# Kernel tuning notes

Hardware: AMD Instinct MI355X
Metric: run time of the kernel (lower is better)

The kernel has to match this reference:

```python
import jax, jax.numpy as jnp
import numpy as np

V, H, B, T = 512, 1024, 128, 128
N_STACK = 4      # n_control_stack = n_work_stack = 4
N_OUT = 4        # n_out_sym
ISIN = 4         # isinstance_dim
ZERO_OFF = 1e-6  # self.zero_offset


def _norm(x):
    n = jnp.linalg.norm(x, axis=-1, keepdims=True)
    return x / jnp.maximum(n, 1e-12)


def nl(x, W):
    # NormalizedLinear: L2-normalize input rows and weight rows, then linear (no bias)
    return _norm(x) @ _norm(W).T


def stack_pop(S, p):
    # hard pop: read at pointer, move pointer down; stack contents unchanged
    read = jnp.einsum('bnv,bn->bv', S, p)
    return read, jnp.roll(p, -1, axis=1)


def stack_hard_push(S, p, v):
    p2 = jnp.roll(p, 1, axis=1)
    S2 = S * (1.0 - p2[..., None]) + v[:, None, :] * p2[..., None]
    return S2, p2


def stack_soft_op(S, p, sharpen, push, pop, nop, val):
    # NTM-style blended push/pop/noop followed by pointer sharpening w^g / sum(w^g)
    p_push = jnp.roll(p, 1, axis=1)
    S_push = S * (1.0 - p_push[..., None]) + val[:, None, :] * p_push[..., None]
    p_pop = jnp.roll(p, -1, axis=1)
    new_p = push[:, None] * p_push + pop[:, None] * p_pop + nop[:, None] * p
    new_S = push[:, None, None] * S_push + (pop + nop)[:, None, None] * S
    sp = jnp.maximum(new_p, 0.0) ** sharpen
    new_p = sp / (sp.sum(axis=1, keepdims=True) + 1e-12)
    return new_S, new_p


def setup_inputs() -> dict:
    key = jax.random.key(0)
    ks = jax.random.split(key, 24)
    sv = 1.0 / np.sqrt(V)
    sh = 1.0 / np.sqrt(H)
    si = 1.0 / np.sqrt(ISIN)
    d = {}
    d['x'] = jax.random.normal(ks[0], (B, T, V), jnp.float32)
    d['W_isin1'] = jax.random.normal(ks[1], (ISIN, V), jnp.float32) * sv
    d['W_isin2'] = jax.random.normal(ks[2], (V, ISIN), jnp.float32) * si
    # 3 gate heads per stack (push, pop, null), stacked on leading axis
    d['cop_W1'] = jax.random.normal(ks[3], (3, H, V), jnp.float32) * sv
    d['cop_b1'] = jax.random.normal(ks[4], (3, H), jnp.float32) * sv
    d['cop_W2'] = jax.random.normal(ks[5], (3, H), jnp.float32) * sh
    d['cop_b2'] = jax.random.normal(ks[6], (3,), jnp.float32) * sh
    d['wop_W1'] = jax.random.normal(ks[7], (3, H, V), jnp.float32) * sv
    d['wop_b1'] = jax.random.normal(ks[8], (3, H), jnp.float32) * sv
    d['wop_W2'] = jax.random.normal(ks[9], (3, H), jnp.float32) * sh
    d['wop_b2'] = jax.random.normal(ks[10], (3,), jnp.float32) * sh
    d['ctrl_W1'] = jax.random.normal(ks[11], (H, V), jnp.float32) * sv
    d['ctrl_W2'] = jax.random.normal(ks[12], (V, H), jnp.float32) * sh
    d['work_W1'] = jax.random.normal(ks[13], (H, V), jnp.float32) * sv
    d['work_W2'] = jax.random.normal(ks[14], (V, H), jnp.float32) * sh
    d['sel_W1'] = jax.random.normal(ks[15], (H, V), jnp.float32) * sv
    d['sel_W2'] = jax.random.normal(ks[16], (N_OUT + 1, H), jnp.float32) * sh
    d['out_sym'] = jax.random.normal(ks[17], (N_OUT, V), jnp.float32)
    d['stack_init_vec'] = jax.random.normal(ks[18], (V,), jnp.float32)
    d['control_sharp'] = jnp.array([2.0], jnp.float32)  # INIT_SHARPEN
    d['work_sharp'] = jnp.array([2.0], jnp.float32)
    return d


def reference(x, W_isin1, W_isin2, cop_W1, cop_b1, cop_W2, cop_b2,
              wop_W1, wop_b1, wop_W2, wop_b2,
              ctrl_W1, ctrl_W2, work_W1, work_W2,
              sel_W1, sel_W2, out_sym, stack_init_vec,
              control_sharp, work_sharp):
    b = x.shape[0]
    S0 = jnp.full((b, N_STACK, V), ZERO_OFF, x.dtype)
    p0 = jnp.zeros((b, N_STACK), x.dtype).at[:, 0].set(1.0)
    init_v = jnp.broadcast_to(stack_init_vec, (b, V))
    cS, cp = stack_hard_push(S0, p0, init_v)
    wS, wp = stack_hard_push(S0, p0, init_v)

    def gates(xy, W1, b1, W2, b2):
        # Sequential(mul, Linear(V,H), Softmax, Linear(H,1), Sigmoid) x3 heads
        h = jax.nn.softmax(jnp.einsum('bv,ghv->gbh', xy, W1) + b1[:, None, :], axis=-1)
        return jax.nn.sigmoid(jnp.einsum('gbh,gh->gb', h, W2) + b2[:, None])  # [3,b]

    def step(carry, inp):
        cS, cp, wS, wp = carry
        control, cp = stack_pop(cS, cp)
        work, wp = stack_pop(wS, wp)
        typ = jnp.tanh(nl(jax.nn.softmax(jax.nn.relu(nl(inp, W_isin1)), axis=-1), W_isin2))
        xy = control * typ
        cg = gates(xy, cop_W1, cop_b1, cop_W2, cop_b2)  # push, pop, null
        wg = gates(xy, wop_W1, wop_b1, wop_W2, wop_b2)
        new_control = jnp.tanh(nl(jax.nn.relu(nl(xy, ctrl_W1)), ctrl_W2))
        new_work = jnp.tanh(nl(jax.nn.relu(nl(work * inp * typ, work_W1)), work_W2))
        sel = jax.nn.softmax(jax.nn.relu(nl(control * work * typ, sel_W1)) @ sel_W2.T, axis=-1)
        options = jnp.concatenate(
            [work[:, None, :], jnp.broadcast_to(out_sym, (inp.shape[0], N_OUT, V))], axis=1)
        out = jnp.einsum('bn,bnv->bv', sel, options)
        cS, cp = stack_soft_op(cS, cp, control_sharp, cg[0], cg[1], cg[2], new_control)
        wS, wp = stack_soft_op(wS, wp, work_sharp, wg[0], wg[1], wg[2], new_work)
        return (cS, cp, wS, wp), out

    _, outs = jax.lax.scan(step, (cS, cp, wS, wp), jnp.swapaxes(x, 0, 1))
    return jnp.swapaxes(outs, 0, 1)  # [B, T, V]
```

## Files before the change

kernel.cpp:

```cpp
#include <hip/hip_runtime.h>
#include <math.h>


#define BB 128
#define TT 128
#define VV 512
#define HH 1024

struct Params {
  const float *x, *Wisin1, *Wisin2, *copW1, *copb1, *copW2, *copb2,
              *wopW1, *wopb1, *wopW2, *wopb2, *ctrlW1, *ctrlW2, *workW1, *workW2,
              *selW1, *selW2, *osym, *initv, *csharp, *wsharp;
  float *cS, *cp, *wS, *wp, *wvec, *xy, *wxy, *sxy, *ixy, *iwxy, *isxy,
        *zP, *kbP, *invW, *out;
};

__device__ inline float block_sum(float v, volatile float* sc) {
#pragma unroll
  for (int off = 32; off; off >>= 1) v += __shfl_down(v, off, 64);
  __syncthreads();
  if ((threadIdx.x & 63) == 0) sc[threadIdx.x >> 6] = v;
  __syncthreads();
  return sc[0] + sc[1] + sc[2] + sc[3];
}

__device__ inline void block_softdot(float& m, float& s, float& w, volatile float* sc) {
#pragma unroll
  for (int off = 32; off; off >>= 1) {
    float m2 = __shfl_down(m, off, 64);
    float s2 = __shfl_down(s, off, 64);
    float w2 = __shfl_down(w, off, 64);
    float M = fmaxf(m, m2);
    float e1 = __expf(m - M), e2 = __expf(m2 - M);
    s = s * e1 + s2 * e2;
    w = w * e1 + w2 * e2;
    m = M;
  }
  __syncthreads();
  if ((threadIdx.x & 63) == 0) {
    int wid = threadIdx.x >> 6;
    sc[wid * 3 + 0] = m; sc[wid * 3 + 1] = s; sc[wid * 3 + 2] = w;
  }
  __syncthreads();
  float M = sc[0], S = sc[1], W = sc[2];
#pragma unroll
  for (int i = 1; i < 4; ++i) {
    float m2 = sc[i * 3], s2 = sc[i * 3 + 1], w2 = sc[i * 3 + 2];
    float nm = fmaxf(M, m2);
    float e1 = __expf(M - nm), e2 = __expf(m2 - nm);
    S = S * e1 + s2 * e2; W = W * e1 + w2 * e2; M = nm;
  }
  m = M; s = S; w = W;
}

__global__ __launch_bounds__(256) void Knorm(Params P) {
  int row = blockIdx.x * 4 + (threadIdx.x >> 6);
  if (row >= 4612) return;
  int lane = threadIdx.x & 63;
  const float* src; int K; int dst;
  if (row < 4)        { src = P.Wisin1 + row * 512;            K = 512;  dst = row; }
  else if (row < 516) { int v = row - 4;    src = P.Wisin2 + v * 4;    K = 4;    dst = 4 + v; }
  else if (row < 1540){ int h = row - 516;  src = P.ctrlW1 + h * 512;  K = 512;  dst = 516 + h; }
  else if (row < 2052){ int v = row - 1540; src = P.ctrlW2 + v * 1024; K = 1024; dst = 1540 + v; }
  else if (row < 3076){ int h = row - 2052; src = P.workW1 + h * 512;  K = 512;  dst = 2052 + h; }
  else if (row < 3588){ int v = row - 3076; src = P.workW2 + v * 1024; K = 1024; dst = 3076 + v; }
  else                { int h = row - 3588; src = P.selW1 + h * 512;   K = 512;  dst = 3588 + h; }
  float s = 0.f;
  for (int k = lane; k < K; k += 64) { float x = src[k]; s += x * x; }
#pragma unroll
  for (int off = 32; off; off >>= 1) s += __shfl_down(s, off, 64);
  if (lane == 0) P.invW[dst] = 1.f / fmaxf(sqrtf(s), 1e-12f);
}

__device__ void prep_step(const Params& P, int b, int tn,
                          const float pcn[4], const float pwn[4],
                          const float newC[4][2], const float newW[4][2],
                          volatile float* sc) {
  int tid = threadIdx.x;
  if (tid == 0) {
#pragma unroll
    for (int n = 0; n < 4; ++n) {
      P.cp[b * 4 + n] = pcn[(n + 1) & 3];
      P.wp[b * 4 + n] = pwn[(n + 1) & 3];
    }
  }
  float ctl[2], wrk[2], inp[2];
#pragma unroll
  for (int i = 0; i < 2; ++i) {
    int v = tid + i * 256;
    float c = 0.f, w = 0.f;
#pragma unroll
    for (int n = 0; n < 4; ++n) { c += pcn[n] * newC[n][i]; w += pwn[n] * newW[n][i]; }
    ctl[i] = c; wrk[i] = w;
    P.wvec[b * 512 + v] = w;
    inp[i] = P.x[(b * TT + tn) * 512 + v];
  }
  float r0 = inp[0] * inp[0] + inp[1] * inp[1];
  float d[4];
#pragma unroll
  for (int j = 0; j < 4; ++j)
    d[j] = inp[0] * P.Wisin1[j * 512 + tid] + inp[1] * P.Wisin1[j * 512 + tid + 256];
  r0 = block_sum(r0, sc);
#pragma unroll
  for (int j = 0; j < 4; ++j) d[j] = block_sum(d[j], sc);
  float inv_in = 1.f / fmaxf(sqrtf(r0), 1e-12f);
  float a[4];
#pragma unroll
  for (int j = 0; j < 4; ++j) a[j] = fmaxf(d[j] * inv_in * P.invW[j], 0.f);
  float mx = fmaxf(fmaxf(a[0], a[1]), fmaxf(a[2], a[3]));
  float e[4], es = 0.f;
#pragma unroll
  for (int j = 0; j < 4; ++j) { e[j] = __expf(a[j] - mx); es += e[j]; }
  float q[4], qs = 0.f;
#pragma unroll
  for (int j = 0; j < 4; ++j) { q[j] = e[j] / es; qs += q[j] * q[j]; }
  float qi = 1.f / fmaxf(sqrtf(qs), 1e-12f);
  float qn[4];
#pragma unroll
  for (int j = 0; j < 4; ++j) qn[j] = q[j] * qi;

  float xys = 0.f, wxs = 0.f, sxs = 0.f;
#pragma unroll
  for (int i = 0; i < 2; ++i) {
    int v = tid + i * 256;
    float dq = 0.f;
#pragma unroll
    for (int j = 0; j < 4; ++j) dq += qn[j] * P.Wisin2[v * 4 + j];
    float typ = tanhf(dq * P.invW[4 + v]);
    float xyv = ctl[i] * typ;
    float wxv = wrk[i] * inp[i] * typ;
    float sxv = ctl[i] * wrk[i] * typ;
    P.xy[b * 512 + v] = xyv;
    P.wxy[b * 512 + v] = wxv;
    P.sxy[b * 512 + v] = sxv;
    xys += xyv * xyv; wxs += wxv * wxv; sxs += sxv * sxv;
  }
  xys = block_sum(xys, sc);
  wxs = block_sum(wxs, sc);
  sxs = block_sum(sxs, sc);
  if (tid == 0) {
    P.ixy[b]  = 1.f / fmaxf(sqrtf(xys), 1e-12f);
    P.iwxy[b] = 1.f / fmaxf(sqrtf(wxs), 1e-12f);
    P.isxy[b] = 1.f / fmaxf(sqrtf(sxs), 1e-12f);
  }
}

__global__ __launch_bounds__(256) void K0(Params P) {
  __shared__ float sc[16];
  int b = blockIdx.x, tid = threadIdx.x;
  float newC[4][2], newW[4][2];
#pragma unroll
  for (int i = 0; i < 2; ++i) {
    int v = tid + i * 256;
    float iv = P.initv[v];
#pragma unroll
    for (int n = 0; n < 4; ++n) {
      float val = (n == 1) ? iv : 1e-6f;
      P.cS[(b * 4 + n) * 512 + v] = val;
      P.wS[(b * 4 + n) * 512 + v] = val;
      newC[n][i] = val; newW[n][i] = val;
    }
  }
  float p0[4] = {0.f, 1.f, 0.f, 0.f};
  __syncthreads();
  prep_step(P, b, 0, p0, p0, newC, newW, sc);
}

__global__ __launch_bounds__(256) void KA(Params P) {
  int w = blockIdx.x;
  int m = w >> 4, ks = (w >> 3) & 1, ct = w & 7;
  const float* X = (m <= 6) ? P.xy : (m == 7 ? P.wxy : P.sxy);
  const float* W;
  if (m < 3)      W = P.copW1 + m * (1024 * 512);
  else if (m < 6) W = P.wopW1 + (m - 3) * (1024 * 512);
  else if (m == 6) W = P.ctrlW1;
  else if (m == 7) W = P.workW1;
  else             W = P.selW1;
  int h0 = ct * 128, k0 = ks * 256;
  __shared__ float xt[32][132];
  __shared__ float wt[32][132];
  float acc[8][8];
#pragma unroll
  for (int j = 0; j < 8; ++j)
#pragma unroll
    for (int i = 0; i < 8; ++i) acc[j][i] = 0.f;
  int cg = threadIdx.x & 15, rg = threadIdx.x >> 4;
  for (int kc = 0; kc < 256; kc += 32) {
#pragma unroll
    for (int i = 0; i < 16; ++i) {
      int flat = i * 256 + threadIdx.x;
      int r = flat >> 5, k = flat & 31;
      xt[k][r] = X[r * 512 + k0 + kc + k];
      wt[k][r] = W[(h0 + r) * 512 + k0 + kc + k];
    }
    __syncthreads();
    for (int k = 0; k < 32; ++k) {
      float a[8], bb[8];
      *(float4*)&a[0] = *(const float4*)&xt[k][rg * 8];
      *(float4*)&a[4] = *(const float4*)&xt[k][rg * 8 + 4];
      *(float4*)&bb[0] = *(const float4*)&wt[k][cg * 8];
      *(float4*)&bb[4] = *(const float4*)&wt[k][cg * 8 + 4];
#pragma unroll
      for (int j = 0; j < 8; ++j)
#pragma unroll
        for (int i = 0; i < 8; ++i) acc[j][i] = fmaf(a[j], bb[i], acc[j][i]);
    }
    __syncthreads();
  }
#pragma unroll
  for (int j = 0; j < 8; ++j) {
    int r = rg * 8 + j;
    float* dst = P.zP + ((m * 2 + ks) * 128 + r) * 1024 + h0 + cg * 8;
    float4 v0 = make_float4(acc[j][0], acc[j][1], acc[j][2], acc[j][3]);
    float4 v1 = make_float4(acc[j][4], acc[j][5], acc[j][6], acc[j][7]);
    *(float4*)&dst[0] = v0;
    *(float4*)&dst[4] = v1;
  }
}

__global__ __launch_bounds__(128) void KB(Params P) {
  int w = blockIdx.x;
  int ks = w & 7, tile = w >> 3;
  int zm = (tile < 8) ? 6 : (tile < 16 ? 7 : 8);
  int colbase = (tile < 16) ? tile * 64 : 1024;
  int k0 = ks * 128;
  __shared__ float at[32][132];
  __shared__ float wt2[32][68];
  float acc[8][8];
#pragma unroll
  for (int j = 0; j < 8; ++j)
#pragma unroll
    for (int i = 0; i < 8; ++i) acc[j][i] = 0.f;
  int cg = threadIdx.x & 7, rg = threadIdx.x >> 3;
  const float* zb0 = P.zP + (zm * 2) * (128 * 1024);
  const float* zb1 = zb0 + 128 * 1024;
  const float* ix = (zm == 6) ? P.ixy : (zm == 7 ? P.iwxy : P.isxy);
  int ioff = (zm == 6) ? 516 : (zm == 7 ? 2052 : 3588);
  for (int kc = 0; kc < 128; kc += 32) {
#pragma unroll
    for (int i = 0; i < 32; ++i) {
      int flat = i * 128 + threadIdx.x;
      int r = flat >> 5, k = flat & 31;
      int h = k0 + kc + k;
      float z = zb0[r * 1024 + h] + zb1[r * 1024 + h];
      at[k][r] = fmaxf(z * (ix[r] * P.invW[ioff + h]), 0.f);
    }
#pragma unroll
    for (int i = 0; i < 16; ++i) {
      int flat = i * 128 + threadIdx.x;
      int c = flat >> 5, k = flat & 31;
      int h = k0 + kc + k;
      float val;
      if (tile < 8)       val = P.ctrlW2[(tile * 64 + c) * 1024 + h];
      else if (tile < 16) val = P.workW2[((tile - 8) * 64 + c) * 1024 + h];
      else                val = (c < 5) ? P.selW2[c * 1024 + h] : 0.f;
      wt2[k][c] = val;
    }
    __syncthreads();
    for (int k = 0; k < 32; ++k) {
      float a[8], bb[8];
      *(float4*)&a[0] = *(const float4*)&at[k][rg * 8];
      *(float4*)&a[4] = *(const float4*)&at[k][rg * 8 + 4];
      *(float4*)&bb[0] = *(const float4*)&wt2[k][cg * 8];
      *(float4*)&bb[4] = *(const float4*)&wt2[k][cg * 8 + 4];
#pragma unroll
      for (int j = 0; j < 8; ++j)
#pragma unroll
        for (int i = 0; i < 8; ++i) acc[j][i] = fmaf(a[j], bb[i], acc[j][i]);
    }
    __syncthreads();
  }
#pragma unroll
  for (int j = 0; j < 8; ++j) {
    int r = rg * 8 + j;
    int col = colbase + cg * 8;
    if (col + 8 <= 1032) {
      float* dst = P.kbP + (ks * 128 + r) * 1032 + col;
      float4 v0 = make_float4(acc[j][0], acc[j][1], acc[j][2], acc[j][3]);
      float4 v1 = make_float4(acc[j][4], acc[j][5], acc[j][6], acc[j][7]);
      *(float4*)&dst[0] = v0;
      *(float4*)&dst[4] = v1;
    }
  }
}

__global__ __launch_bounds__(256) void KC(Params P, int t) {
  __shared__ float sc[16];
  __shared__ float shg[6];
  __shared__ float shsel[5];
  int b = blockIdx.x, tid = threadIdx.x;

  for (int g = 0; g < 6; ++g) {
    const float* zb0 = P.zP + (g * 2) * (128 * 1024) + b * 1024;
    const float* zb1 = zb0 + 128 * 1024;
    const float* b1 = (g < 3) ? (P.copb1 + g * 1024) : (P.wopb1 + (g - 3) * 1024);
    const float* W2 = (g < 3) ? (P.copW2 + g * 1024) : (P.wopW2 + (g - 3) * 1024);
    float m = -INFINITY, s = 0.f, wacc = 0.f;
    for (int h = tid; h < 1024; h += 256) {
      float z = zb0[h] + zb1[h] + b1[h];
      float w2h = W2[h];
      if (z > m) {
        float e = __expf(m - z);
        s = s * e + 1.f;
        wacc = wacc * e + w2h;
        m = z;
      } else {
        float e = __expf(z - m);
        s += e;
        wacc = fmaf(w2h, e, wacc);
      }
    }
    block_softdot(m, s, wacc, sc);
    if (tid == 0) {
      float b2 = (g < 3) ? P.copb2[g] : P.wopb2[g - 3];
      float zz = wacc / s + b2;
      shg[g] = 1.f / (1.f + __expf(-zz));
    }
  }

  float s6 = 0.f, s7 = 0.f;
  {
    const float* z60 = P.zP + 12 * (128 * 1024) + b * 1024;
    const float* z61 = z60 + 128 * 1024;
    const float* z70 = P.zP + 14 * (128 * 1024) + b * 1024;
    const float* z71 = z70 + 128 * 1024;
    float ix = P.ixy[b], iw = P.iwxy[b];
    for (int h = tid; h < 1024; h += 256) {
      float z6 = (z60[h] + z61[h]) * (ix * P.invW[516 + h]);
      float r6 = fmaxf(z6, 0.f); s6 += r6 * r6;
      float z7 = (z70[h] + z71[h]) * (iw * P.invW[2052 + h]);
      float r7 = fmaxf(z7, 0.f); s7 += r7 * r7;
    }
  }
  s6 = block_sum(s6, sc);
  s7 = block_sum(s7, sc);
  float inv_n0 = 1.f / fmaxf(sqrtf(s6), 1e-12f);
  float inv_n1 = 1.f / fmaxf(sqrtf(s7), 1e-12f);

  if (tid < 5) {
    float l = 0.f;
    for (int ks = 0; ks < 8; ++ks) l += P.kbP[(ks * 128 + b) * 1032 + 1024 + tid];
    shsel[tid] = l;
  }
  __syncthreads();
  if (tid == 0) {
    float mx = shsel[0];
    for (int j = 1; j < 5; ++j) mx = fmaxf(mx, shsel[j]);
    float es = 0.f, e[5];
    for (int j = 0; j < 5; ++j) { e[j] = __expf(shsel[j] - mx); es += e[j]; }
    for (int j = 0; j < 5; ++j) shsel[j] = e[j] / es;
  }
  __syncthreads();

  float ncv[2], nwv[2];
#pragma unroll
  for (int i = 0; i < 2; ++i) {
    int v = tid + i * 256;
    float a = 0.f, c = 0.f;
    for (int ks = 0; ks < 8; ++ks) {
      const float* row = P.kbP + (ks * 128 + b) * 1032;
      a += row[v];
      c += row[512 + v];
    }
    ncv[i] = tanhf(a * inv_n0 * P.invW[1540 + v]);
    nwv[i] = tanhf(c * inv_n1 * P.invW[3076 + v]);
    float wv = P.wvec[b * 512 + v];
    float o = shsel[0] * wv;
#pragma unroll
    for (int j = 0; j < 4; ++j) o += shsel[1 + j] * P.osym[j * 512 + v];
    P.out[(b * TT + t) * 512 + v] = o;
  }

  float pc[4], pw[4];
#pragma unroll
  for (int n = 0; n < 4; ++n) { pc[n] = P.cp[b * 4 + n]; pw[n] = P.wp[b * 4 + n]; }
  float G0 = shg[0], G1 = shg[1], G2 = shg[2];
  float Hh0 = shg[3], Hh1 = shg[4], Hh2 = shg[5];
  float ppc[4], ppoc[4], ppw[4], ppow[4], npc[4], npw[4];
#pragma unroll
  for (int n = 0; n < 4; ++n) {
    ppc[n] = pc[(n + 3) & 3]; ppoc[n] = pc[(n + 1) & 3];
    ppw[n] = pw[(n + 3) & 3]; ppow[n] = pw[(n + 1) & 3];
    npc[n] = G0 * ppc[n] + G1 * ppoc[n] + G2 * pc[n];
    npw[n] = Hh0 * ppw[n] + Hh1 * ppow[n] + Hh2 * pw[n];
  }
  float shc = P.csharp[0], shw = P.wsharp[0];
  float pcn[4], pwn[4], sumc = 0.f, sumw = 0.f;
#pragma unroll
  for (int n = 0; n < 4; ++n) {
    float sp = powf(fmaxf(npc[n], 0.f), shc);
    float sq = powf(fmaxf(npw[n], 0.f), shw);
    pcn[n] = sp; pwn[n] = sq; sumc += sp; sumw += sq;
  }
  sumc += 1e-12f; sumw += 1e-12f;
#pragma unroll
  for (int n = 0; n < 4; ++n) { pcn[n] /= sumc; pwn[n] /= sumw; }

  float newC[4][2], newW[4][2];
#pragma unroll
  for (int i = 0; i < 2; ++i) {
    int v = tid + i * 256;
#pragma unroll
    for (int n = 0; n < 4; ++n) {
      float s = P.cS[(b * 4 + n) * 512 + v];
      float t1 = G0 * (s * (1.f - ppc[n]) + ncv[i] * ppc[n]) + (G1 + G2) * s;
      newC[n][i] = t1;
      P.cS[(b * 4 + n) * 512 + v] = t1;
      float s2 = P.wS[(b * 4 + n) * 512 + v];
      float t2 = Hh0 * (s2 * (1.f - ppw[n]) + nwv[i] * ppw[n]) + (Hh1 + Hh2) * s2;
      newW[n][i] = t2;
      P.wS[(b * 4 + n) * 512 + v] = t2;
    }
  }
  __syncthreads();
  if (t + 1 < TT) prep_step(P, b, t + 1, pcn, pwn, newC, newW, sc);
}

extern "C" void kernel_launch(void* const* d_in, const int* in_sizes, int n_in,
                              void* d_out, int out_size, void* d_ws, size_t ws_size,
                              hipStream_t stream) {
  Params P;
  const float* const* in = (const float* const*)d_in;
  P.x = in[0]; P.Wisin1 = in[1]; P.Wisin2 = in[2];
  P.copW1 = in[3]; P.copb1 = in[4]; P.copW2 = in[5]; P.copb2 = in[6];
  P.wopW1 = in[7]; P.wopb1 = in[8]; P.wopW2 = in[9]; P.wopb2 = in[10];
  P.ctrlW1 = in[11]; P.ctrlW2 = in[12]; P.workW1 = in[13]; P.workW2 = in[14];
  P.selW1 = in[15]; P.selW2 = in[16]; P.osym = in[17]; P.initv = in[18];
  P.csharp = in[19]; P.wsharp = in[20];

  float* w = (float*)d_ws;
  P.cS = w;   w += 128 * 4 * 512;
  P.cp = w;   w += 128 * 4;
  P.wS = w;   w += 128 * 4 * 512;
  P.wp = w;   w += 128 * 4;
  P.wvec = w; w += 128 * 512;
  P.xy = w;   w += 128 * 512;
  P.wxy = w;  w += 128 * 512;
  P.sxy = w;  w += 128 * 512;
  P.ixy = w;  w += 128;
  P.iwxy = w; w += 128;
  P.isxy = w; w += 128;
  P.zP = w;   w += 9 * 2 * 128 * 1024;
  P.kbP = w;  w += 8 * 128 * 1032;
  P.invW = w; w += 4612;
  P.out = (float*)d_out;

  Knorm<<<1153, 256, 0, stream>>>(P);
  K0<<<128, 256, 0, stream>>>(P);
  for (int t = 0; t < TT; ++t) {
    KA<<<144, 256, 0, stream>>>(P);
    KB<<<136, 128, 0, stream>>>(P);
    KC<<<128, 256, 0, stream>>>(P, t);
  }
}
```

Baseline: 19.69 ms.

## Use split-bf16 MFMA for the first-layer GEMM and drop split-K partials

Before the time loop, the nine first-layer weight matrices are converted once into high and low bf16 halves. Each step also writes the activations as hi/lo bf16 pairs. KA now computes the GEMM with 16x16x32 bf16 MFMA using three products (hh, hl, lh), which approximates fp32 accuracy on matrix cores instead of scalar FMA. The split-K partial buffers are removed, so KB and KC read a single z buffer. The cost is extra conversion work and traffic for the hi/lo buffers, plus a small loss of accuracy from dropping the lo*lo term.

```diff
diff --git a/kernel.cpp b/kernel.cpp
--- a/kernel.cpp
+++ b/kernel.cpp
@@ -6,6 +6,9 @@
 #define TT 128
 #define VV 512
 #define HH 1024
+
+typedef __attribute__((ext_vector_type(8))) short bf16x8;
+typedef __attribute__((ext_vector_type(4))) float f32x4;
 
 struct Params {
   const float *x, *Wisin1, *Wisin2, *copW1, *copb1, *copW2, *copb2,
@@ -13,7 +16,18 @@
               *selW1, *selW2, *osym, *initv, *csharp, *wsharp;
   float *cS, *cp, *wS, *wp, *wvec, *xy, *wxy, *sxy, *ixy, *iwxy, *isxy,
         *zP, *kbP, *invW, *out;
+  unsigned short *xyh, *xyl, *wxyh, *wxyl, *sxyh, *sxyl, *Wbh, *Wbl;
 };
+
+__device__ inline unsigned short f2bf(float x) {
+  union { float f; unsigned u; } c; c.f = x;
+  unsigned r = (c.u + 0x7FFFu + ((c.u >> 16) & 1u)) >> 16;
+  return (unsigned short)r;
+}
+__device__ inline float bf2f(unsigned short h) {
+  union { unsigned u; float f; } c; c.u = ((unsigned)h) << 16;
+  return c.f;
+}
 
 __device__ inline float block_sum(float v, volatile float* sc) {
 #pragma unroll
@@ -72,6 +86,23 @@
   if (lane == 0) P.invW[dst] = 1.f / fmaxf(sqrtf(s), 1e-12f);
 }
 
+__global__ __launch_bounds__(256) void Kconv(Params P) {
+  const int total = 9 * 1024 * 512;
+  for (int e = blockIdx.x * 256 + threadIdx.x; e < total; e += gridDim.x * 256) {
+    int m = e >> 19, rem = e & ((1 << 19) - 1);
+    const float* base;
+    if (m < 3)       base = P.copW1 + (m << 19);
+    else if (m < 6)  base = P.wopW1 + ((m - 3) << 19);
+    else if (m == 6) base = P.ctrlW1;
+    else if (m == 7) base = P.workW1;
+    else             base = P.selW1;
+    float v = base[rem];
+    unsigned short h = f2bf(v);
+    P.Wbh[e] = h;
+    P.Wbl[e] = f2bf(v - bf2f(h));
+  }
+}
+
 __device__ void prep_step(const Params& P, int b, int tn,
                           const float pcn[4], const float pwn[4],
                           const float newC[4][2], const float newW[4][2],
@@ -133,6 +164,10 @@
     P.xy[b * 512 + v] = xyv;
     P.wxy[b * 512 + v] = wxv;
     P.sxy[b * 512 + v] = sxv;
+    unsigned short hh;
+    hh = f2bf(xyv); P.xyh[b * 512 + v] = hh; P.xyl[b * 512 + v] = f2bf(xyv - bf2f(hh));
+    hh = f2bf(wxv); P.wxyh[b * 512 + v] = hh; P.wxyl[b * 512 + v] = f2bf(wxv - bf2f(hh));
+    hh = f2bf(sxv); P.sxyh[b * 512 + v] = hh; P.sxyl[b * 512 + v] = f2bf(sxv - bf2f(hh));
     xys += xyv * xyv; wxs += wxv * wxv; sxs += sxv * sxv;
   }
   xys = block_sum(xys, sc);
@@ -167,55 +202,80 @@
 }
 
 __global__ __launch_bounds__(256) void KA(Params P) {
-  int w = blockIdx.x;
-  int m = w >> 4, ks = (w >> 3) & 1, ct = w & 7;
-  const float* X = (m <= 6) ? P.xy : (m == 7 ? P.wxy : P.sxy);
-  const float* W;
-  if (m < 3)      W = P.copW1 + m * (1024 * 512);
-  else if (m < 6) W = P.wopW1 + (m - 3) * (1024 * 512);
-  else if (m == 6) W = P.ctrlW1;
-  else if (m == 7) W = P.workW1;
-  else             W = P.selW1;
-  int h0 = ct * 128, k0 = ks * 256;
-  __shared__ float xt[32][132];
-  __shared__ float wt[32][132];
-  float acc[8][8];
-#pragma unroll
-  for (int j = 0; j < 8; ++j)
-#pragma unroll
-    for (int i = 0; i < 8; ++i) acc[j][i] = 0.f;
-  int cg = threadIdx.x & 15, rg = threadIdx.x >> 4;
-  for (int kc = 0; kc < 256; kc += 32) {
-#pragma unroll
-    for (int i = 0; i < 16; ++i) {
-      int flat = i * 256 + threadIdx.x;
-      int r = flat >> 5, k = flat & 31;
-      xt[k][r] = X[r * 512 + k0 + kc + k];
-      wt[k][r] = W[(h0 + r) * 512 + k0 + kc + k];
-    }
+  int blk = blockIdx.x;
+  int m_id = blk >> 4, ct = blk & 15;
+  int h0 = ct * 64;
+  const unsigned short *Xh, *Xl;
+  if (m_id <= 6)      { Xh = P.xyh;  Xl = P.xyl; }
+  else if (m_id == 7) { Xh = P.wxyh; Xl = P.wxyl; }
+  else                { Xh = P.sxyh; Xl = P.sxyl; }
+  __shared__ unsigned short lds[24576];
+  int tid = threadIdx.x;
+  int w = tid >> 6, lane = tid & 63, wm = w >> 1, wn = w & 1;
+  f32x4 acc[4][2];
+#pragma unroll
+  for (int mf = 0; mf < 4; ++mf)
+#pragma unroll
+    for (int nf = 0; nf < 2; ++nf) acc[mf][nf] = (f32x4)(0.0f);
+  const int wbase = (m_id * 1024 + h0) * 512;
+  for (int kb = 0; kb < 8; ++kb) {
+    int k0 = kb * 64;
     __syncthreads();
-    for (int k = 0; k < 32; ++k) {
-      float a[8], bb[8];
-      *(float4*)&a[0] = *(const float4*)&xt[k][rg * 8];
-      *(float4*)&a[4] = *(const float4*)&xt[k][rg * 8 + 4];
-      *(float4*)&bb[0] = *(const float4*)&wt[k][cg * 8];
-      *(float4*)&bb[4] = *(const float4*)&wt[k][cg * 8 + 4];
-#pragma unroll
-      for (int j = 0; j < 8; ++j)
-#pragma unroll
-        for (int i = 0; i < 8; ++i) acc[j][i] = fmaf(a[j], bb[i], acc[j][i]);
+#pragma unroll
+    for (int it = 0; it < 4; ++it) {
+      int c = it * 256 + tid;
+      int r = c >> 3, o = c & 7;
+      int so = (r << 9) + k0 + (o << 3);
+      int doff = (((r >> 4) * 2 + (o >> 2)) * 64 + ((r & 15) | ((o & 3) << 4))) * 8;
+      *(uint4*)&lds[doff]        = *(const uint4*)&Xh[so];
+      *(uint4*)&lds[8192 + doff] = *(const uint4*)&Xl[so];
+    }
+#pragma unroll
+    for (int it = 0; it < 2; ++it) {
+      int c = it * 256 + tid;
+      int hh = c >> 3, o = c & 7;
+      int so = wbase + (hh << 9) + k0 + (o << 3);
+      int doff = (((hh >> 4) * 2 + (o >> 2)) * 64 + ((hh & 15) | ((o & 3) << 4))) * 8;
+      *(uint4*)&lds[16384 + doff] = *(const uint4*)&P.Wbh[so];
+      *(uint4*)&lds[20480 + doff] = *(const uint4*)&P.Wbl[so];
     }
     __syncthreads();
-  }
-#pragma unroll
-  for (int j = 0; j < 8; ++j) {
-    int r = rg * 8 + j;
-    float* dst = P.zP + ((m * 2 + ks) * 128 + r) * 1024 + h0 + cg * 8;
-    float4 v0 = make_float4(acc[j][0], acc[j][1], acc[j][2], acc[j][3]);
-    float4 v1 = make_float4(acc[j][4], acc[j][5], acc[j][6], acc[j][7]);
-    *(float4*)&dst[0] = v0;
-    *(float4*)&dst[4] = v1;
-  }
+#pragma unroll
+    for (int kc = 0; kc < 2; ++kc) {
+      bf16x8 ah[4], al[4], bh[2], bl[2];
+#pragma unroll
+      for (int mf = 0; mf < 4; ++mf) {
+        int off = (((wm * 4 + mf) * 2 + kc) * 64 + lane) * 8;
+        ah[mf] = *(bf16x8*)&lds[off];
+        al[mf] = *(bf16x8*)&lds[8192 + off];
+      }
+#pragma unroll
+      for (int nf = 0; nf < 2; ++nf) {
+        int off = (((wn * 2 + nf) * 2 + kc) * 64 + lane) * 8;
+        bh[nf] = *(bf16x8*)&lds[16384 + off];
+        bl[nf] = *(bf16x8*)&lds[20480 + off];
+      }
+#pragma unroll
+      for (int mf = 0; mf < 4; ++mf)
+#pragma unroll
+        for (int nf = 0; nf < 2; ++nf) {
+          acc[mf][nf] = __builtin_amdgcn_mfma_f32_16x16x32_bf16(ah[mf], bh[nf], acc[mf][nf], 0, 0, 0);
+          acc[mf][nf] = __builtin_amdgcn_mfma_f32_16x16x32_bf16(ah[mf], bl[nf], acc[mf][nf], 0, 0, 0);
+          acc[mf][nf] = __builtin_amdgcn_mfma_f32_16x16x32_bf16(al[mf], bh[nf], acc[mf][nf], 0, 0, 0);
+        }
+    }
+  }
+  float* zdst = P.zP + m_id * 131072;
+#pragma unroll
+  for (int mf = 0; mf < 4; ++mf)
+#pragma unroll
+    for (int nf = 0; nf < 2; ++nf)
+#pragma unroll
+      for (int r = 0; r < 4; ++r) {
+        int row = wm * 64 + mf * 16 + ((lane >> 4) << 2) + r;
+        int col = h0 + wn * 32 + nf * 16 + (lane & 15);
+        zdst[(row << 10) + col] = acc[mf][nf][r];
+      }
 }
 
 __global__ __launch_bounds__(128) void KB(Params P) {
@@ -232,8 +292,7 @@
 #pragma unroll
     for (int i = 0; i < 8; ++i) acc[j][i] = 0.f;
   int cg = threadIdx.x & 7, rg = threadIdx.x >> 3;
-  const float* zb0 = P.zP + (zm * 2) * (128 * 1024);
-  const float* zb1 = zb0 + 128 * 1024;
+  const float* zb0 = P.zP + zm * 131072;
   const float* ix = (zm == 6) ? P.ixy : (zm == 7 ? P.iwxy : P.isxy);
   int ioff = (zm == 6) ? 516 : (zm == 7 ? 2052 : 3588);
   for (int kc = 0; kc < 128; kc += 32) {
@@ -242,7 +301,7 @@
       int flat = i * 128 + threadIdx.x;
       int r = flat >> 5, k = flat & 31;
       int h = k0 + kc + k;
-      float z = zb0[r * 1024 + h] + zb1[r * 1024 + h];
+      float z = zb0[r * 1024 + h];
       at[k][r] = fmaxf(z * (ix[r] * P.invW[ioff + h]), 0.f);
     }
 #pragma unroll
@@ -291,13 +350,12 @@
   int b = blockIdx.x, tid = threadIdx.x;
 
   for (int g = 0; g < 6; ++g) {
-    const float* zb0 = P.zP + (g * 2) * (128 * 1024) + b * 1024;
-    const float* zb1 = zb0 + 128 * 1024;
+    const float* zb = P.zP + g * 131072 + b * 1024;
     const float* b1 = (g < 3) ? (P.copb1 + g * 1024) : (P.wopb1 + (g - 3) * 1024);
     const float* W2 = (g < 3) ? (P.copW2 + g * 1024) : (P.wopW2 + (g - 3) * 1024);
     float m = -INFINITY, s = 0.f, wacc = 0.f;
     for (int h = tid; h < 1024; h += 256) {
-      float z = zb0[h] + zb1[h] + b1[h];
+      float z = zb[h] + b1[h];
       float w2h = W2[h];
       if (z > m) {
         float e = __expf(m - z);
@@ -320,15 +378,13 @@
 
   float s6 = 0.f, s7 = 0.f;
   {
-    const float* z60 = P.zP + 12 * (128 * 1024) + b * 1024;
-    const float* z61 = z60 + 128 * 1024;
-    const float* z70 = P.zP + 14 * (128 * 1024) + b * 1024;
-    const float* z71 = z70 + 128 * 1024;
+    const float* z6p = P.zP + 6 * 131072 + b * 1024;
+    const float* z7p = P.zP + 7 * 131072 + b * 1024;
     float ix = P.ixy[b], iw = P.iwxy[b];
     for (int h = tid; h < 1024; h += 256) {
-      float z6 = (z60[h] + z61[h]) * (ix * P.invW[516 + h]);
+      float z6 = z6p[h] * (ix * P.invW[516 + h]);
       float r6 = fmaxf(z6, 0.f); s6 += r6 * r6;
-      float z7 = (z70[h] + z71[h]) * (iw * P.invW[2052 + h]);
+      float z7 = z7p[h] * (iw * P.invW[2052 + h]);
       float r7 = fmaxf(z7, 0.f); s7 += r7 * r7;
     }
   }
@@ -440,12 +496,21 @@
   P.ixy = w;  w += 128;
   P.iwxy = w; w += 128;
   P.isxy = w; w += 128;
-  P.zP = w;   w += 9 * 2 * 128 * 1024;
+  P.zP = w;   w += 9 * 128 * 1024;
   P.kbP = w;  w += 8 * 128 * 1032;
-  P.invW = w; w += 4612;
+  P.invW = w; w += 4616;
+  P.xyh  = (unsigned short*)w; w += 32768;
+  P.xyl  = (unsigned short*)w; w += 32768;
+  P.wxyh = (unsigned short*)w; w += 32768;
+  P.wxyl = (unsigned short*)w; w += 32768;
+  P.sxyh = (unsigned short*)w; w += 32768;
+  P.sxyl = (unsigned short*)w; w += 32768;
+  P.Wbh  = (unsigned short*)w; w += 9 * 1024 * 512 / 2;
+  P.Wbl  = (unsigned short*)w; w += 9 * 1024 * 512 / 2;
   P.out = (float*)d_out;
 
   Knorm<<<1153, 256, 0, stream>>>(P);
+  Kconv<<<4608, 256, 0, stream>>>(P);
   K0<<<128, 256, 0, stream>>>(P);
   for (int t = 0; t < TT; ++t) {
     KA<<<144, 256, 0, stream>>>(P);
```

Result: faster. 16.49 ms (-16.3%).
